# Performance work log

Hardware: AMD Instinct MI355X
Metric: run time of the kernel (lower is better)

Reference implementation:

```python
import jax, jax.numpy as jnp
import numpy as np

DIM = 1024
NUM_HEADS = 16
HEAD_DIM = DIM // NUM_HEADS
B, N_Q, N_KV = 8, 1024, 1024


def setup_inputs() -> dict:
    key = jax.random.key(0)
    ks = jax.random.split(key, 12)
    s = 1.0 / np.sqrt(DIM)
    inp = {
        "query": jax.random.normal(ks[0], (B, N_Q, DIM), jnp.float32),
        "key_value": jax.random.normal(ks[1], (B, N_KV, DIM), jnp.float32),
        "cluster_matrix": jax.random.normal(ks[2], (B, N_Q, N_KV), jnp.float32),
        "Wq": jax.random.uniform(ks[3], (DIM, DIM), jnp.float32, -s, s),
        "bq": jax.random.uniform(ks[4], (DIM,), jnp.float32, -s, s),
        "Wk": jax.random.uniform(ks[5], (DIM, DIM), jnp.float32, -s, s),
        "bk": jax.random.uniform(ks[6], (DIM,), jnp.float32, -s, s),
        "Wv": jax.random.uniform(ks[7], (DIM, DIM), jnp.float32, -s, s),
        "bv": jax.random.uniform(ks[8], (DIM,), jnp.float32, -s, s),
        "Wo": jax.random.uniform(ks[9], (DIM, DIM), jnp.float32, -s, s),
        "bo": jax.random.uniform(ks[10], (DIM,), jnp.float32, -s, s),
    }
    return inp


def reference(query, key_value, cluster_matrix, Wq, bq, Wk, bk, Wv, bv, Wo, bo):
    Bsz, Nq, D = query.shape
    Nkv = key_value.shape[1]
    H, Hd = NUM_HEADS, HEAD_DIM
    # projections (torch Linear: x @ W.T + b)
    Q = (query @ Wq.T + bq).reshape(Bsz, Nq, H, Hd).transpose(0, 2, 1, 3)      # [B,H,Nq,Hd]
    K = (key_value @ Wk.T + bk).reshape(Bsz, Nkv, H, Hd).transpose(0, 2, 1, 3)  # [B,H,Nkv,Hd]
    V = (key_value @ Wv.T + bv).reshape(Bsz, Nkv, H, Hd).transpose(0, 2, 1, 3)
    scale = 1.0 / jnp.sqrt(jnp.asarray(Hd, Q.dtype))
    scores = jnp.einsum("bhqd,bhkd->bhqk", Q, K) * scale + cluster_matrix[:, None]  # [B,H,Nq,Nkv]
    attn_weights = jax.nn.softmax(scores, axis=-1)
    attn_out = jnp.einsum("bhqk,bhkd->bhqd", attn_weights, V)
    attn_out = attn_out.transpose(0, 2, 1, 3).reshape(Bsz, Nq, D)
    updated_query = attn_out @ Wo.T + bo
    attn_matrix = attn_weights.mean(axis=1)  # head-mean [B,Nq,Nkv]
    return updated_query, attn_matrix
```

## Files before the change

### kernel.cpp

```cpp
#include <hip/hip_runtime.h>
#include <stdint.h>
#include <stddef.h>

typedef __attribute__((ext_vector_type(4))) float  f32x4;
typedef __attribute__((ext_vector_type(4))) float  float4v;
typedef __attribute__((ext_vector_type(8))) short  s16x8;
typedef __attribute__((ext_vector_type(4))) short  s16x4;
typedef __attribute__((ext_vector_type(2))) unsigned int u32x2;

#define DEV static __device__ __forceinline__

DEV short f2bf(float f) {
  unsigned u = __builtin_bit_cast(unsigned, f);
  u = u + 0x7fffu + ((u >> 16) & 1u);
  return (short)(u >> 16);
}
DEV float bf2f(short s) {
  unsigned u = ((unsigned)(unsigned short)s) << 16;
  return __builtin_bit_cast(float, u);
}
DEV f32x4 vmax4(f32x4 a, f32x4 b) {
  f32x4 r;
  r[0] = fmaxf(a[0], b[0]); r[1] = fmaxf(a[1], b[1]);
  r[2] = fmaxf(a[2], b[2]); r[3] = fmaxf(a[3], b[3]);
  return r;
}
DEV void gload16(const void* g, void* l) {
  __builtin_amdgcn_global_load_lds((const __attribute__((address_space(1))) void*)g,
                                   (__attribute__((address_space(3))) void*)l, 16, 0, 0);
}

__global__ void cvt4(const float4v* __restrict__ src, s16x4* __restrict__ dst, int n4) {
  int i = blockIdx.x * 256 + threadIdx.x;
  if (i >= n4) return;
  float4v v = src[i];
  s16x4 o; o.x = f2bf(v.x); o.y = f2bf(v.y); o.z = f2bf(v.z); o.w = f2bf(v.w);
  dst[i] = o;
}
__global__ void cvt_dup(const float4v* __restrict__ src, s16x8* __restrict__ dst, int n4) {
  int i = blockIdx.x * 256 + threadIdx.x;
  if (i >= n4) return;
  float4v v = src[i];
  s16x8 o;
  o[0] = f2bf(v.x); o[1] = o[0];
  o[2] = f2bf(v.y); o[3] = o[2];
  o[4] = f2bf(v.z); o[5] = o[4];
  o[6] = f2bf(v.w); o[7] = o[6];
  dst[i] = o;
}

template <int EPI, int KDIM>
__global__ __launch_bounds__(256) void gemm_nt(const short* __restrict__ A,
                                               const short* __restrict__ Bw,
                                               const float* __restrict__ bias,
                                               void* __restrict__ Cp) {
  __shared__ __attribute__((aligned(16))) short As[2][128 * 32];
  __shared__ __attribute__((aligned(16))) short Bs[2][128 * 32];
  const int tid = threadIdx.x;
  const int wg  = blockIdx.x;
  const int swz = (wg & 7) * ((int)gridDim.x >> 3) + (wg >> 3);
  const int bm = swz >> 3, bn = swz & 7;
  const int mbase = bm * 128, nbase = bn * 128;
  const int w = tid >> 6, l = tid & 63;
  const int wm = w >> 1, wn = w & 1;

  auto stage = [&](int buf, int kt) {
#pragma unroll
    for (int j = 0; j < 2; ++j) {
      int cb  = w * 128 + j * 64;
      int ci  = cb + l;
      int row = ci >> 2, cc = ci & 3;
      int c   = cc ^ ((row >> 1) & 3);
      gload16(A  + (size_t)(mbase + row) * KDIM + kt * 32 + c * 8, &As[buf][cb * 8]);
      gload16(Bw + (size_t)(nbase + row) * KDIM + kt * 32 + c * 8, &Bs[buf][cb * 8]);
    }
  };

  f32x4 acc[4][4];
#pragma unroll
  for (int i = 0; i < 4; ++i)
#pragma unroll
    for (int j = 0; j < 4; ++j) acc[i][j] = (f32x4){0.f, 0.f, 0.f, 0.f};

  const int KSTEPS = KDIM / 32;
  stage(0, 0);
  for (int kt = 0; kt < KSTEPS; ++kt) {
    __syncthreads();
    if (kt + 1 < KSTEPS) stage((kt + 1) & 1, kt + 1);
    const int buf = kt & 1;
    s16x8 af[4], bf[4];
    const int g = l >> 4;
#pragma unroll
    for (int i = 0; i < 4; ++i) {
      int ra = wm * 64 + i * 16 + (l & 15);
      int pa = g ^ ((ra >> 1) & 3);
      af[i] = *(const s16x8*)&As[buf][ra * 32 + pa * 8];
      int rb = wn * 64 + i * 16 + (l & 15);
      int pb = g ^ ((rb >> 1) & 3);
      bf[i] = *(const s16x8*)&Bs[buf][rb * 32 + pb * 8];
    }
#pragma unroll
    for (int i = 0; i < 4; ++i)
#pragma unroll
      for (int j = 0; j < 4; ++j)
        acc[i][j] = __builtin_amdgcn_mfma_f32_16x16x32_bf16(af[i], bf[j], acc[i][j], 0, 0, 0);
  }

  float bj[4];
#pragma unroll
  for (int j = 0; j < 4; ++j) bj[j] = bias[nbase + wn * 64 + j * 16 + (l & 15)];
#pragma unroll
  for (int i = 0; i < 4; ++i) {
#pragma unroll
    for (int j = 0; j < 4; ++j) {
      int m0 = mbase + wm * 64 + i * 16 + (l >> 4) * 4;
      int n  = nbase + wn * 64 + j * 16 + (l & 15);
      if constexpr (EPI == 0) {
        short* C16 = (short*)Cp;
#pragma unroll
        for (int jj = 0; jj < 4; ++jj)
          C16[(size_t)(m0 + jj) * 1024 + n] = f2bf(acc[i][j][jj] + bj[j]);
      } else if constexpr (EPI == 1) {
        float* Cf = (float*)Cp;
#pragma unroll
        for (int jj = 0; jj < 4; ++jj)
          Cf[(size_t)(m0 + jj) * 1024 + n] = acc[i][j][jj] + bj[j];
      } else {
        short* C16 = (short*)Cp;
        int bb = m0 >> 10, kv = m0 & 1023;
        s16x4 o;
#pragma unroll
        for (int jj = 0; jj < 4; ++jj) o[jj] = f2bf(acc[i][j][jj] + bj[j]);
        *(s16x4*)&C16[((size_t)(bb * 1024 + n)) * 1024 + kv] = o;
      }
    }
  }
}

__global__ __launch_bounds__(512, 2) void attn_fused3(const short* __restrict__ Qp,
                                                      const short* __restrict__ Kp,
                                                      const short* __restrict__ Vt,
                                                      const float* __restrict__ cluster,
                                                      short* __restrict__ AO2,
                                                      float* __restrict__ Amean) {
  constexpr int PSTR = 1032;
  __shared__ __attribute__((aligned(16))) short Pbuf[32 * PSTR];
  __shared__ float mlbuf[32][20];
  __shared__ __attribute__((aligned(16))) f32x4 obuf[4][2][16][4];
  const int tid = threadIdx.x;
  const int b = blockIdx.y, qt = blockIdx.x;
  const int w = tid >> 6, l = tid & 63;
  const int li = l & 15, g = l >> 4;
  const int wkv = w * 128;
  const int db = w & 3, kvh = w >> 2;
  const float LOG2E = 1.4426950408889634f;
  const float scaleL = 0.125f * LOG2E;

  const size_t qrow0 = (size_t)(b * 1024 + qt * 32);
  const size_t krow0 = (size_t)(b * 1024);

  f32x4 clv[2][8], macc[2][8];
#pragma unroll
  for (int qcb = 0; qcb < 2; ++qcb) {
    const float* clp = cluster + (qrow0 + qcb * 16 + li) * 1024 + wkv + 4 * g;
#pragma unroll
    for (int kb = 0; kb < 8; ++kb) {
      f32x4 cl = *(const f32x4*)(clp + kb * 16);
      clv[qcb][kb] = cl * LOG2E;
      macc[qcb][kb] = (f32x4){0.f, 0.f, 0.f, 0.f};
    }
  }

  for (int h = 0; h < 16; ++h) {
    s16x8 qf[2][2];
#pragma unroll
    for (int qcb = 0; qcb < 2; ++qcb)
#pragma unroll
      for (int kc = 0; kc < 2; ++kc)
        qf[qcb][kc] = *(const s16x8*)&Qp[(qrow0 + qcb * 16 + li) * 1024 + h * 64 + kc * 32 + g * 8];

    f32x4 acc[2][8];
#pragma unroll
    for (int a = 0; a < 2; ++a)
#pragma unroll
      for (int kb = 0; kb < 8; ++kb) acc[a][kb] = (f32x4){0.f, 0.f, 0.f, 0.f};

#pragma unroll
    for (int quarter = 0; quarter < 4; ++quarter) {
      s16x8 kf[4];
#pragma unroll
      for (int i = 0; i < 4; ++i) {
        int kb = quarter * 2 + (i >> 1), kc = i & 1;
        kf[i] = *(const s16x8*)&Kp[(krow0 + wkv + kb * 16 + li) * 1024 + h * 64 + kc * 32 + g * 8];
      }
#pragma unroll
      for (int i = 0; i < 4; ++i) {
        int kb = quarter * 2 + (i >> 1), kc = i & 1;
#pragma unroll
        for (int qcb = 0; qcb < 2; ++qcb)
          acc[qcb][kb] = __builtin_amdgcn_mfma_f32_16x16x32_bf16(kf[i], qf[qcb][kc], acc[qcb][kb], 0, 0, 0);
      }
    }

    float mw[2], lw[2];
#pragma unroll
    for (int qcb = 0; qcb < 2; ++qcb) {
#pragma unroll
      for (int kb = 0; kb < 8; ++kb)
        acc[qcb][kb] = acc[qcb][kb] * scaleL + clv[qcb][kb];
      f32x4 mx = acc[qcb][0];
#pragma unroll
      for (int kb = 1; kb < 8; ++kb) mx = vmax4(mx, acc[qcb][kb]);
      float m = fmaxf(fmaxf(mx[0], mx[1]), fmaxf(mx[2], mx[3]));
      m = fmaxf(m, __shfl_xor(m, 16, 64));
      m = fmaxf(m, __shfl_xor(m, 32, 64));
      f32x4 s4 = (f32x4){0.f, 0.f, 0.f, 0.f};
#pragma unroll
      for (int kb = 0; kb < 8; ++kb) {
        f32x4 e;
#pragma unroll
        for (int jj = 0; jj < 4; ++jj) e[jj] = __builtin_amdgcn_exp2f(acc[qcb][kb][jj] - m);
        acc[qcb][kb] = e;
        s4 += e;
      }
      float s = (s4[0] + s4[1]) + (s4[2] + s4[3]);
      s += __shfl_xor(s, 16, 64);
      s += __shfl_xor(s, 32, 64);
      mw[qcb] = m; lw[qcb] = s;
    }
    if (l < 16) {
#pragma unroll
      for (int qcb = 0; qcb < 2; ++qcb) {
        mlbuf[qcb * 16 + l][2 * w]     = mw[qcb];
        mlbuf[qcb * 16 + l][2 * w + 1] = lw[qcb];
      }
    }
    __syncthreads();

#pragma unroll
    for (int qcb = 0; qcb < 2; ++qcb) {
      const int q = qcb * 16 + li;
      float m = mlbuf[q][0];
#pragma unroll
      for (int j = 1; j < 8; ++j) m = fmaxf(m, mlbuf[q][2 * j]);
      float lt = 0.f;
#pragma unroll
      for (int j = 0; j < 8; ++j) lt += mlbuf[q][2 * j + 1] * __builtin_amdgcn_exp2f(mlbuf[q][2 * j] - m);
      const float c = __builtin_amdgcn_exp2f(mw[qcb] - m) / lt;
#pragma unroll
      for (int kb = 0; kb < 8; ++kb) {
        f32x4 p = acc[qcb][kb] * c;
        macc[qcb][kb] += p;
        unsigned u0 = (unsigned)(unsigned short)f2bf(p[0]) | ((unsigned)(unsigned short)f2bf(p[1]) << 16);
        unsigned u1 = (unsigned)(unsigned short)f2bf(p[2]) | ((unsigned)(unsigned short)f2bf(p[3]) << 16);
        u32x2 uu; uu[0] = u0; uu[1] = u1;
        *(u32x2*)&Pbuf[q * PSTR + wkv + kb * 16 + 4 * g] = uu;
      }
    }
    __syncthreads();

    f32x4 o0a = (f32x4){0.f,0.f,0.f,0.f}, o0b = o0a, o1a = o0a, o1b = o0a;
    {
      const short* vb = Vt + ((size_t)((b * 16 + h) * 64 + db * 16 + li)) * 1024 + kvh * 512 + g * 8;
      const short* p0 = &Pbuf[li * PSTR + kvh * 512 + g * 8];
      const short* p1 = &Pbuf[(16 + li) * PSTR + kvh * 512 + g * 8];
#pragma unroll
      for (int kc = 0; kc < 16; kc += 2) {
        s16x8 vfa = *(const s16x8*)(vb + kc * 32);
        s16x8 vfb = *(const s16x8*)(vb + kc * 32 + 32);
        s16x8 pa0 = *(const s16x8*)(p0 + kc * 32);
        s16x8 pb0 = *(const s16x8*)(p0 + kc * 32 + 32);
        s16x8 pa1 = *(const s16x8*)(p1 + kc * 32);
        s16x8 pb1 = *(const s16x8*)(p1 + kc * 32 + 32);
        o0a = __builtin_amdgcn_mfma_f32_16x16x32_bf16(pa0, vfa, o0a, 0, 0, 0);
        o1a = __builtin_amdgcn_mfma_f32_16x16x32_bf16(pa1, vfa, o1a, 0, 0, 0);
        o0b = __builtin_amdgcn_mfma_f32_16x16x32_bf16(pb0, vfb, o0b, 0, 0, 0);
        o1b = __builtin_amdgcn_mfma_f32_16x16x32_bf16(pb1, vfb, o1b, 0, 0, 0);
      }
    }
    f32x4 of0 = o0a + o0b, of1 = o1a + o1b;
    if (kvh == 1) obuf[db][0][li][g] = of0;
    else          obuf[db][1][li][g] = of1;
    __syncthreads();
    {
      f32x4 of = (kvh == 0) ? (of0 + obuf[db][0][li][g]) : (of1 + obuf[db][1][li][g]);
      const int qb = kvh;
#pragma unroll
      for (int jj = 0; jj < 4; ++jj) {
        int q = qb * 16 + g * 4 + jj;
        int d = db * 16 + li;
        float x = of[jj];
        short hi = f2bf(x);
        short lo = f2bf(x - bf2f(hi));
        *(unsigned*)&AO2[(qrow0 + q) * 2048 + (size_t)(h * 64 + d) * 2] =
            (unsigned)(unsigned short)hi | ((unsigned)(unsigned short)lo << 16);
      }
    }
  }

#pragma unroll
  for (int qcb = 0; qcb < 2; ++qcb)
#pragma unroll
    for (int kb = 0; kb < 8; ++kb)
      *(f32x4*)&Amean[(qrow0 + qcb * 16 + li) * 1024 + wkv + kb * 16 + 4 * g] = macc[qcb][kb] * 0.0625f;
}

extern "C" void kernel_launch(void* const* d_in, const int* in_sizes, int n_in,
                              void* d_out, int out_size, void* d_ws, size_t ws_size,
                              hipStream_t stream) {
  (void)in_sizes; (void)n_in; (void)out_size; (void)ws_size;
  const float* query     = (const float*)d_in[0];
  const float* key_value = (const float*)d_in[1];
  const float* cluster   = (const float*)d_in[2];
  const float* Wq = (const float*)d_in[3];
  const float* bq = (const float*)d_in[4];
  const float* Wk = (const float*)d_in[5];
  const float* bk = (const float*)d_in[6];
  const float* Wv = (const float*)d_in[7];
  const float* bv = (const float*)d_in[8];
  const float* Wo = (const float*)d_in[9];
  const float* bo = (const float*)d_in[10];

  char* ws = (char*)d_ws;
  short* qb  = (short*)(ws);
  short* kvb = (short*)(ws + 16777216);
  short* Wqb = (short*)(ws + 33554432);
  short* Wkb = (short*)(ws + 35651584);
  short* Wvb = (short*)(ws + 37748736);
  short* Wo2 = (short*)(ws + 39845888);
  short* Qp  = (short*)(ws + 44040192);
  short* Kp  = (short*)(ws + 60817408);
  short* Vtp = (short*)(ws + 77594624);
  short* AO2 = (short*)(ws + 94371840);

  float* out_uq = (float*)d_out;
  float* out_am = (float*)d_out + 8388608;

  cvt4<<<8192, 256, 0, stream>>>((const float4v*)query,     (s16x4*)qb,  2097152);
  cvt4<<<8192, 256, 0, stream>>>((const float4v*)key_value, (s16x4*)kvb, 2097152);
  cvt4<<<1024, 256, 0, stream>>>((const float4v*)Wq, (s16x4*)Wqb, 262144);
  cvt4<<<1024, 256, 0, stream>>>((const float4v*)Wk, (s16x4*)Wkb, 262144);
  cvt4<<<1024, 256, 0, stream>>>((const float4v*)Wv, (s16x4*)Wvb, 262144);
  cvt_dup<<<1024, 256, 0, stream>>>((const float4v*)Wo, (s16x8*)Wo2, 262144);

  gemm_nt<0, 1024><<<512, 256, 0, stream>>>(qb,  Wqb, bq, Qp);
  gemm_nt<0, 1024><<<512, 256, 0, stream>>>(kvb, Wkb, bk, Kp);
  gemm_nt<2, 1024><<<512, 256, 0, stream>>>(kvb, Wvb, bv, Vtp);

  attn_fused3<<<dim3(32, 8), 512, 0, stream>>>(Qp, Kp, Vtp, cluster, AO2, out_am);

  gemm_nt<1, 2048><<<512, 256, 0, stream>>>(AO2, Wo2, bo, out_uq);
}
```

Before: 496.1 us.

## Halve attention query tile to 16 rows to double grid size and occupancy

Each attention block now handles 16 query rows instead of 32, doubling the grid to 512 blocks and raising launch bounds to allow more resident blocks per CU. Register and LDS use per block shrink, and the PV stage is restructured so each wave accumulates one query tile over four interleaved accumulators. The aim is better latency hiding and CU fill. In exchange, K and V tiles are re-read twice as often per query and the MFMA reuse of each K fragment is halved.

```diff
diff --git a/kernel.cpp b/kernel.cpp
--- a/kernel.cpp
+++ b/kernel.cpp
@@ -137,16 +137,16 @@
   }
 }
 
-__global__ __launch_bounds__(512, 2) void attn_fused3(const short* __restrict__ Qp,
+__global__ __launch_bounds__(512, 4) void attn_fused4(const short* __restrict__ Qp,
                                                       const short* __restrict__ Kp,
                                                       const short* __restrict__ Vt,
                                                       const float* __restrict__ cluster,
                                                       short* __restrict__ AO2,
                                                       float* __restrict__ Amean) {
   constexpr int PSTR = 1032;
-  __shared__ __attribute__((aligned(16))) short Pbuf[32 * PSTR];
-  __shared__ float mlbuf[32][20];
-  __shared__ __attribute__((aligned(16))) f32x4 obuf[4][2][16][4];
+  __shared__ __attribute__((aligned(16))) short Pbuf[16 * PSTR];
+  __shared__ float mlbuf[16][20];
+  __shared__ __attribute__((aligned(16))) f32x4 obuf[4][16][4];
   const int tid = threadIdx.x;
   const int b = blockIdx.y, qt = blockIdx.x;
   const int w = tid >> 6, l = tid & 63;
@@ -156,34 +156,29 @@
   const float LOG2E = 1.4426950408889634f;
   const float scaleL = 0.125f * LOG2E;
 
-  const size_t qrow0 = (size_t)(b * 1024 + qt * 32);
+  const size_t qrow0 = (size_t)(b * 1024 + qt * 16);
   const size_t krow0 = (size_t)(b * 1024);
 
-  f32x4 clv[2][8], macc[2][8];
-#pragma unroll
-  for (int qcb = 0; qcb < 2; ++qcb) {
-    const float* clp = cluster + (qrow0 + qcb * 16 + li) * 1024 + wkv + 4 * g;
+  f32x4 clv[8], macc[8];
+  {
+    const float* clp = cluster + (qrow0 + li) * 1024 + wkv + 4 * g;
 #pragma unroll
     for (int kb = 0; kb < 8; ++kb) {
       f32x4 cl = *(const f32x4*)(clp + kb * 16);
-      clv[qcb][kb] = cl * LOG2E;
-      macc[qcb][kb] = (f32x4){0.f, 0.f, 0.f, 0.f};
+      clv[kb] = cl * LOG2E;
+      macc[kb] = (f32x4){0.f, 0.f, 0.f, 0.f};
     }
   }
 
   for (int h = 0; h < 16; ++h) {
-    s16x8 qf[2][2];
-#pragma unroll
-    for (int qcb = 0; qcb < 2; ++qcb)
-#pragma unroll
-      for (int kc = 0; kc < 2; ++kc)
-        qf[qcb][kc] = *(const s16x8*)&Qp[(qrow0 + qcb * 16 + li) * 1024 + h * 64 + kc * 32 + g * 8];
-
-    f32x4 acc[2][8];
-#pragma unroll
-    for (int a = 0; a < 2; ++a)
-#pragma unroll
-      for (int kb = 0; kb < 8; ++kb) acc[a][kb] = (f32x4){0.f, 0.f, 0.f, 0.f};
+    s16x8 qf[2];
+#pragma unroll
+    for (int kc = 0; kc < 2; ++kc)
+      qf[kc] = *(const s16x8*)&Qp[(qrow0 + li) * 1024 + h * 64 + kc * 32 + g * 8];
+
+    f32x4 acc[8];
+#pragma unroll
+    for (int kb = 0; kb < 8; ++kb) acc[kb] = (f32x4){0.f, 0.f, 0.f, 0.f};
 
 #pragma unroll
     for (int quarter = 0; quarter < 4; ++quarter) {
@@ -196,21 +191,18 @@
 #pragma unroll
       for (int i = 0; i < 4; ++i) {
         int kb = quarter * 2 + (i >> 1), kc = i & 1;
-#pragma unroll
-        for (int qcb = 0; qcb < 2; ++qcb)
-          acc[qcb][kb] = __builtin_amdgcn_mfma_f32_16x16x32_bf16(kf[i], qf[qcb][kc], acc[qcb][kb], 0, 0, 0);
-      }
-    }
-
-    float mw[2], lw[2];
-#pragma unroll
-    for (int qcb = 0; qcb < 2; ++qcb) {
+        acc[kb] = __builtin_amdgcn_mfma_f32_16x16x32_bf16(kf[i], qf[kc], acc[kb], 0, 0, 0);
+      }
+    }
+
+    float mw, lw;
+    {
 #pragma unroll
       for (int kb = 0; kb < 8; ++kb)
-        acc[qcb][kb] = acc[qcb][kb] * scaleL + clv[qcb][kb];
-      f32x4 mx = acc[qcb][0];
-#pragma unroll
-      for (int kb = 1; kb < 8; ++kb) mx = vmax4(mx, acc[qcb][kb]);
+        acc[kb] = acc[kb] * scaleL + clv[kb];
+      f32x4 mx = acc[0];
+#pragma unroll
+      for (int kb = 1; kb < 8; ++kb) mx = vmax4(mx, acc[kb]);
       float m = fmaxf(fmaxf(mx[0], mx[1]), fmaxf(mx[2], mx[3]));
       m = fmaxf(m, __shfl_xor(m, 16, 64));
       m = fmaxf(m, __shfl_xor(m, 32, 64));
@@ -219,38 +211,34 @@
       for (int kb = 0; kb < 8; ++kb) {
         f32x4 e;
 #pragma unroll
-        for (int jj = 0; jj < 4; ++jj) e[jj] = __builtin_amdgcn_exp2f(acc[qcb][kb][jj] - m);
-        acc[qcb][kb] = e;
+        for (int jj = 0; jj < 4; ++jj) e[jj] = __builtin_amdgcn_exp2f(acc[kb][jj] - m);
+        acc[kb] = e;
         s4 += e;
       }
       float s = (s4[0] + s4[1]) + (s4[2] + s4[3]);
       s += __shfl_xor(s, 16, 64);
       s += __shfl_xor(s, 32, 64);
-      mw[qcb] = m; lw[qcb] = s;
+      mw = m; lw = s;
     }
     if (l < 16) {
-#pragma unroll
-      for (int qcb = 0; qcb < 2; ++qcb) {
-        mlbuf[qcb * 16 + l][2 * w]     = mw[qcb];
-        mlbuf[qcb * 16 + l][2 * w + 1] = lw[qcb];
-      }
+      mlbuf[l][2 * w]     = mw;
+      mlbuf[l][2 * w + 1] = lw;
     }
     __syncthreads();
 
-#pragma unroll
-    for (int qcb = 0; qcb < 2; ++qcb) {
-      const int q = qcb * 16 + li;
+    {
+      const int q = li;
       float m = mlbuf[q][0];
 #pragma unroll
       for (int j = 1; j < 8; ++j) m = fmaxf(m, mlbuf[q][2 * j]);
       float lt = 0.f;
 #pragma unroll
       for (int j = 0; j < 8; ++j) lt += mlbuf[q][2 * j + 1] * __builtin_amdgcn_exp2f(mlbuf[q][2 * j] - m);
-      const float c = __builtin_amdgcn_exp2f(mw[qcb] - m) / lt;
+      const float c = __builtin_amdgcn_exp2f(mw - m) / lt;
 #pragma unroll
       for (int kb = 0; kb < 8; ++kb) {
-        f32x4 p = acc[qcb][kb] * c;
-        macc[qcb][kb] += p;
+        f32x4 p = acc[kb] * c;
+        macc[kb] += p;
         unsigned u0 = (unsigned)(unsigned short)f2bf(p[0]) | ((unsigned)(unsigned short)f2bf(p[1]) << 16);
         unsigned u1 = (unsigned)(unsigned short)f2bf(p[2]) | ((unsigned)(unsigned short)f2bf(p[3]) << 16);
         u32x2 uu; uu[0] = u0; uu[1] = u1;
@@ -259,35 +247,34 @@
     }
     __syncthreads();
 
-    f32x4 o0a = (f32x4){0.f,0.f,0.f,0.f}, o0b = o0a, o1a = o0a, o1b = o0a;
+    f32x4 oa = (f32x4){0.f,0.f,0.f,0.f}, ob = oa, oc = oa, od = oa;
     {
       const short* vb = Vt + ((size_t)((b * 16 + h) * 64 + db * 16 + li)) * 1024 + kvh * 512 + g * 8;
       const short* p0 = &Pbuf[li * PSTR + kvh * 512 + g * 8];
-      const short* p1 = &Pbuf[(16 + li) * PSTR + kvh * 512 + g * 8];
-#pragma unroll
-      for (int kc = 0; kc < 16; kc += 2) {
-        s16x8 vfa = *(const s16x8*)(vb + kc * 32);
-        s16x8 vfb = *(const s16x8*)(vb + kc * 32 + 32);
-        s16x8 pa0 = *(const s16x8*)(p0 + kc * 32);
-        s16x8 pb0 = *(const s16x8*)(p0 + kc * 32 + 32);
-        s16x8 pa1 = *(const s16x8*)(p1 + kc * 32);
-        s16x8 pb1 = *(const s16x8*)(p1 + kc * 32 + 32);
-        o0a = __builtin_amdgcn_mfma_f32_16x16x32_bf16(pa0, vfa, o0a, 0, 0, 0);
-        o1a = __builtin_amdgcn_mfma_f32_16x16x32_bf16(pa1, vfa, o1a, 0, 0, 0);
-        o0b = __builtin_amdgcn_mfma_f32_16x16x32_bf16(pb0, vfb, o0b, 0, 0, 0);
-        o1b = __builtin_amdgcn_mfma_f32_16x16x32_bf16(pb1, vfb, o1b, 0, 0, 0);
-      }
-    }
-    f32x4 of0 = o0a + o0b, of1 = o1a + o1b;
-    if (kvh == 1) obuf[db][0][li][g] = of0;
-    else          obuf[db][1][li][g] = of1;
+#pragma unroll
+      for (int kc = 0; kc < 16; kc += 4) {
+        s16x8 vf0 = *(const s16x8*)(vb + (kc + 0) * 32);
+        s16x8 pf0 = *(const s16x8*)(p0 + (kc + 0) * 32);
+        s16x8 vf1 = *(const s16x8*)(vb + (kc + 1) * 32);
+        s16x8 pf1 = *(const s16x8*)(p0 + (kc + 1) * 32);
+        s16x8 vf2 = *(const s16x8*)(vb + (kc + 2) * 32);
+        s16x8 pf2 = *(const s16x8*)(p0 + (kc + 2) * 32);
+        s16x8 vf3 = *(const s16x8*)(vb + (kc + 3) * 32);
+        s16x8 pf3 = *(const s16x8*)(p0 + (kc + 3) * 32);
+        oa = __builtin_amdgcn_mfma_f32_16x16x32_bf16(pf0, vf0, oa, 0, 0, 0);
+        ob = __builtin_amdgcn_mfma_f32_16x16x32_bf16(pf1, vf1, ob, 0, 0, 0);
+        oc = __builtin_amdgcn_mfma_f32_16x16x32_bf16(pf2, vf2, oc, 0, 0, 0);
+        od = __builtin_amdgcn_mfma_f32_16x16x32_bf16(pf3, vf3, od, 0, 0, 0);
+      }
+    }
+    f32x4 of = (oa + ob) + (oc + od);
+    if (kvh == 1) obuf[db][li][g] = of;
     __syncthreads();
-    {
-      f32x4 of = (kvh == 0) ? (of0 + obuf[db][0][li][g]) : (of1 + obuf[db][1][li][g]);
-      const int qb = kvh;
+    if (kvh == 0) {
+      of = of + obuf[db][li][g];
 #pragma unroll
       for (int jj = 0; jj < 4; ++jj) {
-        int q = qb * 16 + g * 4 + jj;
+        int q = g * 4 + jj;
         int d = db * 16 + li;
         float x = of[jj];
         short hi = f2bf(x);
@@ -299,10 +286,8 @@
   }
 
 #pragma unroll
-  for (int qcb = 0; qcb < 2; ++qcb)
-#pragma unroll
-    for (int kb = 0; kb < 8; ++kb)
-      *(f32x4*)&Amean[(qrow0 + qcb * 16 + li) * 1024 + wkv + kb * 16 + 4 * g] = macc[qcb][kb] * 0.0625f;
+  for (int kb = 0; kb < 8; ++kb)
+    *(f32x4*)&Amean[(qrow0 + li) * 1024 + wkv + kb * 16 + 4 * g] = macc[kb] * 0.0625f;
 }
 
 extern "C" void kernel_launch(void* const* d_in, const int* in_sizes, int n_in,
@@ -347,7 +332,7 @@
   gemm_nt<0, 1024><<<512, 256, 0, stream>>>(kvb, Wkb, bk, Kp);
   gemm_nt<2, 1024><<<512, 256, 0, stream>>>(kvb, Wvb, bv, Vtp);
 
-  attn_fused3<<<dim3(32, 8), 512, 0, stream>>>(Qp, Kp, Vtp, cluster, AO2, out_am);
+  attn_fused4<<<dim3(64, 8), 512, 0, stream>>>(Qp, Kp, Vtp, cluster, AO2, out_am);
 
   gemm_nt<1, 2048><<<512, 256, 0, stream>>>(AO2, Wo2, bo, out_uq);
 }
```

Result: slower. 673.1 us (+35.7%).
